# Kernel optimization log

Measured on AMD Instinct MI355X. Metric: run time of the kernel, lower is better.

## Reference

```python
import jax, jax.numpy as jnp
import numpy as np

NEG_SLOPE = 0.01  # torch LeakyReLU default
LN_EPS = 1e-5
L2_EPS = 1e-12  # torch F.normalize eps


def setup_inputs() -> dict:
    key = jax.random.key(0)
    ks = jax.random.split(key, 8)
    B, T, N, C = 16, 32, 64, 256
    local_feat = jax.random.normal(ks[0], (B, T, N, C), dtype=jnp.float32)
    global_feat = jax.random.normal(ks[1], (B, C), dtype=jnp.float32)
    pos = jax.random.normal(ks[2], (B, T * N, 3), dtype=jnp.float32)
    adj_w = jax.random.normal(ks[3], (C, C), dtype=jnp.float32) * (1.0 / np.sqrt(C))
    affine_w = jax.random.normal(ks[4], (C, C), dtype=jnp.float32) * np.sqrt(2.0 / C)  # kaiming-ish
    affine_b = jnp.zeros((C,), dtype=jnp.float32)
    ln_g = jnp.ones((C,), dtype=jnp.float32)
    ln_b = jnp.zeros((C,), dtype=jnp.float32)
    return {"local_feat": local_feat, "global_feat": global_feat, "pos": pos,
            "adj_w": adj_w, "affine_w": affine_w, "affine_b": affine_b,
            "ln_g": ln_g, "ln_b": ln_b}


def reference(local_feat, global_feat, pos, adj_w, affine_w, affine_b, ln_g, ln_b):
    B, T, N, C = local_feat.shape
    x = local_feat.reshape(B, T * N, C)  # [B, M, C]
    # L2 normalize along features
    nrm = jnp.sqrt(jnp.sum(x * x, axis=-1, keepdims=True))
    nf = x / jnp.maximum(nrm, L2_EPS)
    # bilinear scores: A = nf @ W @ nf^T  -> [B, M, M]
    A = jnp.einsum('bnc,cd,bmd->bnm', nf, adj_w, nf)
    A = 5.0 * (A - jnp.max(A, axis=-1, keepdims=True))
    A = jax.nn.softmax(A, axis=-1)
    # affine projection (torch Linear: x @ W^T + b)
    h = jnp.einsum('bmc,dc->bmd', x, affine_w) + affine_b
    # aggregation
    h = jnp.einsum('bnm,bmc->bnc', A, h)
    # LayerNorm + LeakyReLU
    mu = jnp.mean(h, axis=-1, keepdims=True)
    var = jnp.mean(jnp.square(h - mu), axis=-1, keepdims=True)
    h = (h - mu) / jnp.sqrt(var + LN_EPS) * ln_g + ln_b
    h = jnp.where(h >= 0, h, NEG_SLOPE * h)
    return h.reshape(B, T, N, C)
```

## Files before the change

### kernel.cpp

```cpp
#include <hip/hip_runtime.h>
#include <hip/hip_bf16.h>
#include <stdint.h>

#define B_  16
#define M_  2048
#define C_  256
#define BM_ 32768

typedef __bf16 bf16x8 __attribute__((ext_vector_type(8)));
typedef __bf16 bf16x2 __attribute__((ext_vector_type(2)));
typedef float  f32x4  __attribute__((ext_vector_type(4)));
typedef float  f32x16 __attribute__((ext_vector_type(16)));
typedef unsigned int uint2v __attribute__((ext_vector_type(2)));

__device__ __forceinline__ unsigned short f2bf(float f) {
    uint32_t u = __builtin_bit_cast(uint32_t, f);
    u += 0x7fffu + ((u >> 16) & 1u);
    return (unsigned short)(u >> 16);
}

__device__ __forceinline__ uint32_t pkbf(float a, float b) {
    bf16x2 t; t[0] = (__bf16)a; t[1] = (__bf16)b;
    return __builtin_bit_cast(uint32_t, t);
}

__device__ __forceinline__ float bf2f(unsigned short u) {
    return __builtin_bit_cast(float, ((uint32_t)u) << 16);
}

__device__ __forceinline__ void gload16(const void* g, void* l) {
    __builtin_amdgcn_global_load_lds(
        (const __attribute__((address_space(1))) void*)g,
        (__attribute__((address_space(3))) void*)l, 16, 0, 0);
}

__device__ __forceinline__ void publish_barrier() {
    asm volatile("s_waitcnt vmcnt(0)" ::: "memory");
    __builtin_amdgcn_sched_barrier(0);
    __syncthreads();
    __builtin_amdgcn_sched_barrier(0);
}

__global__ void prep_weights(const float* __restrict__ adj,
                             const float* __restrict__ affw,
                             unsigned short* __restrict__ adjT5,
                             unsigned short* __restrict__ affwB) {
    int idx = blockIdx.x * 256 + threadIdx.x;
    int d = idx >> 8, c = idx & 255;
    adjT5[d * 256 + c] = f2bf(7.2134752f * adj[c * 256 + d]);
    affwB[idx] = f2bf(affw[idx]);
}

__global__ void l2norm_kernel(const float* __restrict__ x,
                              unsigned short* __restrict__ nf,
                              float* __restrict__ norms) {
    int w = threadIdx.x >> 6, lane = threadIdx.x & 63;
    int row = blockIdx.x * 4 + w;
    const float4 v = *reinterpret_cast<const float4*>(x + (size_t)row * 256 + lane * 4);
    float ss = v.x * v.x + v.y * v.y + v.z * v.z + v.w * v.w;
    #pragma unroll
    for (int m = 1; m < 64; m <<= 1) ss += __shfl_xor(ss, m);
    float nrm = sqrtf(ss);
    float s = 1.0f / fmaxf(nrm, 1e-12f);
    ushort4 o;
    o.x = f2bf(v.x * s); o.y = f2bf(v.y * s); o.z = f2bf(v.z * s); o.w = f2bf(v.w * s);
    *reinterpret_cast<ushort4*>(nf + (size_t)row * 256 + lane * 4) = o;
    if (lane == 0) norms[row] = nrm;
}

__global__ __launch_bounds__(512, 2)
void dual_gemm(const unsigned short* __restrict__ A,
               const unsigned short* __restrict__ B1,
               const unsigned short* __restrict__ B2,
               const float* __restrict__ norms,
               const float* __restrict__ bias,
               unsigned short* __restrict__ outQ,
               unsigned short* __restrict__ outV3) {
    __shared__ unsigned short bb1[256 * 56];
    __shared__ unsigned short bb2[256 * 56];
    int tid = threadIdx.x;
    int w = tid >> 6, lane = tid & 63, g = lane >> 4, r = lane & 15;
    int m0 = blockIdx.x * 128;

    const f32x4 z = {0.f, 0.f, 0.f, 0.f};
    f32x4 accq[16], accv[16];
    #pragma unroll
    for (int i = 0; i < 16; i++) { accq[i] = z; accv[i] = z; }

    for (int dc = 0; dc < 8; dc++) {
        __syncthreads();
        #pragma unroll
        for (int it = 0; it < 2; it++) {
            int n = (w * 2 + it) * 16 + (lane >> 2);
            int t = lane & 3;
            *reinterpret_cast<uint4*>(&bb1[n * 56 + t * 8]) =
                *reinterpret_cast<const uint4*>(B1 + (size_t)n * 256 + dc * 32 + t * 8);
            *reinterpret_cast<uint4*>(&bb2[n * 56 + t * 8]) =
                *reinterpret_cast<const uint4*>(B2 + (size_t)n * 256 + dc * 32 + t * 8);
        }
        __syncthreads();
        bf16x8 af = *reinterpret_cast<const bf16x8*>(
            A + (size_t)(m0 + w * 16 + r) * 256 + dc * 32 + g * 8);
        #pragma unroll
        for (int nf16 = 0; nf16 < 16; nf16++) {
            bf16x8 b1f = *reinterpret_cast<const bf16x8*>(&bb1[(nf16 * 16 + r) * 56 + g * 8]);
            accq[nf16] = __builtin_amdgcn_mfma_f32_16x16x32_bf16(af, b1f, accq[nf16], 0, 0, 0);
            bf16x8 b2f = *reinterpret_cast<const bf16x8*>(&bb2[(nf16 * 16 + r) * 56 + g * 8]);
            accv[nf16] = __builtin_amdgcn_mfma_f32_16x16x32_bf16(af, b2f, accv[nf16], 0, 0, 0);
        }
    }
    #pragma unroll
    for (int nf16 = 0; nf16 < 16; nf16++) {
        int n = nf16 * 16 + r;
        #pragma unroll
        for (int j = 0; j < 4; j++) {
            int m = m0 + w * 16 + g * 4 + j;
            outQ[(size_t)m * 256 + n] = f2bf(accq[nf16][j]);
        }
    }
    int mm = m0 + w * 16 + g * 4;
    int kvblk = mm >> 5;
    int kv0 = mm & 31;
    int jj  = kv0 >> 4;
    int hl2 = (kv0 >> 3) & 1;
    int e0  = kv0 & 7;
    float4 nr = *reinterpret_cast<const float4*>(norms + mm);
    #pragma unroll
    for (int nf16 = 0; nf16 < 16; nf16++) {
        int n = nf16 * 16 + r;
        int cb = n >> 5, mrow = n & 31;
        int slot = (cb * 2 + jj) * 64 + hl2 * 32 + mrow;
        float bv = bias[n];
        ushort4 o;
        o.x = f2bf(accv[nf16][0] * nr.x + bv);
        o.y = f2bf(accv[nf16][1] * nr.y + bv);
        o.z = f2bf(accv[nf16][2] * nr.z + bv);
        o.w = f2bf(accv[nf16][3] * nr.w + bv);
        *reinterpret_cast<ushort4*>(outV3 + (size_t)kvblk * 8192 + slot * 8 + e0) = o;
    }
}

__global__ __launch_bounds__(512, 1)
void flash_kernel(const unsigned short* __restrict__ Q,
                  const unsigned short* __restrict__ K,
                  const unsigned short* __restrict__ V3,
                  const float* __restrict__ gam,
                  const float* __restrict__ bet,
                  float* __restrict__ out) {
    __shared__ __align__(16) char smem[132096];
    const int tid = threadIdx.x;
    const int w = tid >> 6, lane = tid & 63;
    const int wg = w & 3, h = w >> 2;
    const int hl = lane >> 5, m = lane & 31;
    const int blk = blockIdx.x;
    const int b = (blk & 7) * 2 + (blk >> 7);
    const int mblk = (blk >> 3) & 15;
    const int q0 = b * M_ + mblk * 128 + wg * 32;
    const int gtid = wg * 64 + lane;

    char* gbase = smem + h * 65536;

    bf16x8 qf[16];
    #pragma unroll
    for (int ch = 0; ch < 16; ch++)
        qf[ch] = *reinterpret_cast<const bf16x8*>(
            Q + (size_t)(q0 + m) * 256 + ch * 16 + hl * 8);

    const f32x16 z16 = {0,0,0,0, 0,0,0,0, 0,0,0,0, 0,0,0,0};
    f32x16 acc[8];
    #pragma unroll
    for (int cb = 0; cb < 8; cb++) acc[cb] = z16;
    float mmax = 0.0f, lsum = 0.0f;

    const unsigned short* Kb = K + (size_t)(b * M_ + h * 1024) * 256;
    const unsigned short* Vsrc =
        V3 + ((size_t)(b * 64 + h * 32) * 1024 + gtid) * 8;

    auto stageK = [&](int step, int buf) {
        char* kb = gbase + buf * 16384;
        #pragma unroll
        for (int it = 0; it < 4; it++) {
            int s = it * 256 + gtid;
            int n = s >> 5, t = s & 31;
            gload16(Kb + (size_t)(step * 32 + n) * 256 + ((t ^ (n & 7)) * 8),
                    kb + (it * 256 + wg * 64) * 16);
        }
    };
    auto stageV = [&](int step, int buf) {
        char* vb = gbase + 32768 + buf * 16384;
        const unsigned short* src = Vsrc + (size_t)step * 8192;
        #pragma unroll
        for (int it = 0; it < 4; it++) {
            gload16(src + it * 2048, vb + (it * 256 + wg * 64) * 16);
        }
    };

    stageK(0, 0); stageV(0, 0);
    publish_barrier();
    stageK(1, 1); stageV(1, 1);

    #pragma unroll 2
    for (int step = 0; step < 32; step++) {
        const int cur = step & 1;
        char* kb = gbase + cur * 16384;
        char* vb = gbase + 32768 + cur * 16384;

        f32x16 sf = z16;
        __builtin_amdgcn_s_setprio(1);
        #pragma unroll
        for (int ch = 0; ch < 16; ch++) {
            int slot = (ch * 2 + hl) ^ (m & 7);
            bf16x8 kf = *reinterpret_cast<const bf16x8*>(kb + m * 512 + slot * 16);
            sf = __builtin_amdgcn_mfma_f32_32x32x16_bf16(kf, qf[ch], sf, 0, 0, 0);
        }
        __builtin_amdgcn_s_setprio(0);

        float tm = sf[0];
        #pragma unroll
        for (int i = 1; i < 16; i++) tm = fmaxf(tm, sf[i]);
        tm = fmaxf(tm, __shfl_xor(tm, 32));
        if (__any(tm > mmax + 11.0f)) {
            float mn = fmaxf(mmax, tm);
            float corr = exp2f(mmax - mn);
            lsum *= corr;
            #pragma unroll
            for (int cb = 0; cb < 8; cb++) acc[cb] *= corr;
            mmax = mn;
        }
        #pragma unroll
        for (int i = 0; i < 16; i++) {
            sf[i] = exp2f(sf[i] - mmax);
            lsum += sf[i];
        }
        uint32_t pk0 = pkbf(sf[0], sf[1]),   pk1 = pkbf(sf[2], sf[3]);
        uint32_t pk2 = pkbf(sf[4], sf[5]),   pk3 = pkbf(sf[6], sf[7]);
        uint32_t pk4 = pkbf(sf[8], sf[9]),   pk5 = pkbf(sf[10], sf[11]);
        uint32_t pk6 = pkbf(sf[12], sf[13]), pk7 = pkbf(sf[14], sf[15]);
        uint2v r0 = __builtin_amdgcn_permlane32_swap(pk0, pk2, false, false);
        uint2v r1 = __builtin_amdgcn_permlane32_swap(pk1, pk3, false, false);
        uint2v r2 = __builtin_amdgcn_permlane32_swap(pk4, pk6, false, false);
        uint2v r3 = __builtin_amdgcn_permlane32_swap(pk5, pk7, false, false);
        uint4 u0; u0.x = r0[0]; u0.y = r1[0]; u0.z = r0[1]; u0.w = r1[1];
        uint4 u1; u1.x = r2[0]; u1.y = r3[0]; u1.z = r2[1]; u1.w = r3[1];
        bf16x8 pf0 = __builtin_bit_cast(bf16x8, u0);
        bf16x8 pf1 = __builtin_bit_cast(bf16x8, u1);

        __builtin_amdgcn_s_setprio(1);
        #pragma unroll
        for (int cb = 0; cb < 8; cb++) {
            bf16x8 v0 = *reinterpret_cast<const bf16x8*>(
                vb + lane * 16 + (cb * 2 + 0) * 1024);
            acc[cb] = __builtin_amdgcn_mfma_f32_32x32x16_bf16(v0, pf0, acc[cb], 0, 0, 0);
            bf16x8 v1 = *reinterpret_cast<const bf16x8*>(
                vb + lane * 16 + (cb * 2 + 1) * 1024);
            acc[cb] = __builtin_amdgcn_mfma_f32_32x32x16_bf16(v1, pf1, acc[cb], 0, 0, 0);
        }
        __builtin_amdgcn_s_setprio(0);

        publish_barrier();
        if (step + 2 < 32) {
            stageK(step + 2, cur);
            stageV(step + 2, cur);
        }
    }

    publish_barrier();

    lsum += __shfl_xor(lsum, 32);
    float inv = 1.0f / lsum;
    float wgt = lsum * exp2f(mmax);

    unsigned short* mp = (unsigned short*)smem;
    float* mlp = (float*)(smem + 131072);
    if (h == 1) {
        #pragma unroll
        for (int cb = 0; cb < 8; cb++)
            #pragma unroll
            for (int q4 = 0; q4 < 4; q4++) {
                int c0i = cb * 32 + q4 * 8 + 4 * hl;
                uint2 u;
                u.x = pkbf(acc[cb][q4 * 4 + 0] * inv, acc[cb][q4 * 4 + 1] * inv);
                u.y = pkbf(acc[cb][q4 * 4 + 2] * inv, acc[cb][q4 * 4 + 3] * inv);
                *reinterpret_cast<uint2*>(mp + (size_t)wg * 8192 + m * 256 + c0i) = u;
            }
        if (hl == 0) mlp[wg * 32 + m] = wgt;
    }
    __syncthreads();
    if (h == 0) {
        float w1 = mlp[wg * 32 + m];
        float rsw = 1.0f / (wgt + w1);
        float c0 = wgt * rsw * inv;
        float c1 = w1 * rsw;
        float s = 0.0f, ssq = 0.0f;
        #pragma unroll
        for (int cb = 0; cb < 8; cb++)
            #pragma unroll
            for (int q4 = 0; q4 < 4; q4++) {
                int c0i = cb * 32 + q4 * 8 + 4 * hl;
                uint2 u = *reinterpret_cast<const uint2*>(
                    mp + (size_t)wg * 8192 + m * 256 + c0i);
                float p0 = bf2f((unsigned short)(u.x & 0xffff));
                float p1 = bf2f((unsigned short)(u.x >> 16));
                float p2 = bf2f((unsigned short)(u.y & 0xffff));
                float p3 = bf2f((unsigned short)(u.y >> 16));
                float v0 = acc[cb][q4 * 4 + 0] * c0 + p0 * c1;
                float v1 = acc[cb][q4 * 4 + 1] * c0 + p1 * c1;
                float v2 = acc[cb][q4 * 4 + 2] * c0 + p2 * c1;
                float v3 = acc[cb][q4 * 4 + 3] * c0 + p3 * c1;
                acc[cb][q4 * 4 + 0] = v0; acc[cb][q4 * 4 + 1] = v1;
                acc[cb][q4 * 4 + 2] = v2; acc[cb][q4 * 4 + 3] = v3;
                s += (v0 + v1) + (v2 + v3);
                ssq += v0 * v0 + v1 * v1 + v2 * v2 + v3 * v3;
            }
        s   += __shfl_xor(s, 32);
        ssq += __shfl_xor(ssq, 32);
        float mu = s * (1.0f / 256.0f);
        float var = ssq * (1.0f / 256.0f) - mu * mu;
        float rstd = rsqrtf(var + 1e-5f);
        size_t rowoff = (size_t)(q0 + m) * 256;
        #pragma unroll
        for (int cb = 0; cb < 8; cb++)
            #pragma unroll
            for (int q4 = 0; q4 < 4; q4++) {
                int c0i = cb * 32 + q4 * 8 + 4 * hl;
                float4 gg = *reinterpret_cast<const float4*>(gam + c0i);
                float4 bb = *reinterpret_cast<const float4*>(bet + c0i);
                float4 o;
                o.x = (acc[cb][q4 * 4 + 0] - mu) * rstd * gg.x + bb.x;
                o.y = (acc[cb][q4 * 4 + 1] - mu) * rstd * gg.y + bb.y;
                o.z = (acc[cb][q4 * 4 + 2] - mu) * rstd * gg.z + bb.z;
                o.w = (acc[cb][q4 * 4 + 3] - mu) * rstd * gg.w + bb.w;
                o.x = o.x >= 0.f ? o.x : 0.01f * o.x;
                o.y = o.y >= 0.f ? o.y : 0.01f * o.y;
                o.z = o.z >= 0.f ? o.z : 0.01f * o.z;
                o.w = o.w >= 0.f ? o.w : 0.01f * o.w;
                *reinterpret_cast<float4*>(out + rowoff + c0i) = o;
            }
    }
}

extern "C" void kernel_launch(void* const* d_in, const int* in_sizes, int n_in,
                              void* d_out, int out_size, void* d_ws, size_t ws_size,
                              hipStream_t stream) {
    const float* local_feat = (const float*)d_in[0];
    const float* adj_w    = (const float*)d_in[3];
    const float* affine_w = (const float*)d_in[4];
    const float* affine_b = (const float*)d_in[5];
    const float* ln_g     = (const float*)d_in[6];
    const float* ln_b     = (const float*)d_in[7];
    float* out = (float*)d_out;

    char* ws = (char*)d_ws;
    unsigned short* nf    = (unsigned short*)(ws);
    unsigned short* q     = (unsigned short*)(ws + 16777216);
    unsigned short* v3    = (unsigned short*)(ws + 33554432);
    float*          norms = (float*)         (ws + 50331648);
    unsigned short* adjT5 = (unsigned short*)(ws + 50462720);
    unsigned short* affw  = (unsigned short*)(ws + 50593792);

    prep_weights<<<256, 256, 0, stream>>>(adj_w, affine_w, adjT5, affw);
    l2norm_kernel<<<BM_ / 4, 256, 0, stream>>>(local_feat, nf, norms);
    dual_gemm<<<BM_ / 128, 512, 0, stream>>>(nf, adjT5, affw, norms, affine_b, q, v3);
    flash_kernel<<<256, 512, 0, stream>>>(q, nf, v3, ln_g, ln_b, out);
}
```

Measured before the change: 137.0 us.

## Pre-swizzle K into MFMA fragment layout in dual_gemm for linear LDS reads

dual_gemm now writes an extra copy of the normalized features (K) in a blocked fragment layout matching the V3 layout. The flash kernel stages K with the same contiguous per-lane 16-byte loads as V and reads K fragments from LDS with a simple lane*16 + ch*1024 offset, dropping the XOR swizzle address math. The main loop's unroll-2 pragma is also removed. This costs an extra 16 MB global write in dual_gemm, and the new LDS read pattern could bring back bank conflicts.

```diff
diff --git a/kernel.cpp b/kernel.cpp
--- a/kernel.cpp
+++ b/kernel.cpp
@@ -75,7 +75,8 @@
                const float* __restrict__ norms,
                const float* __restrict__ bias,
                unsigned short* __restrict__ outQ,
-               unsigned short* __restrict__ outV3) {
+               unsigned short* __restrict__ outV3,
+               unsigned short* __restrict__ outK3) {
     __shared__ unsigned short bb1[256 * 56];
     __shared__ unsigned short bb2[256 * 56];
     int tid = threadIdx.x;
@@ -86,6 +87,9 @@
     f32x4 accq[16], accv[16];
     #pragma unroll
     for (int i = 0; i < 16; i++) { accq[i] = z; accv[i] = z; }
+
+    int row = m0 + w * 16 + r;
+    int kvblk_r = row >> 5, mrow = row & 31;
 
     for (int dc = 0; dc < 8; dc++) {
         __syncthreads();
@@ -100,7 +104,13 @@
         }
         __syncthreads();
         bf16x8 af = *reinterpret_cast<const bf16x8*>(
-            A + (size_t)(m0 + w * 16 + r) * 256 + dc * 32 + g * 8);
+            A + (size_t)row * 256 + dc * 32 + g * 8);
+        {
+            int ch = dc * 2 + (g >> 1);
+            int khl = g & 1;
+            *reinterpret_cast<bf16x8*>(
+                outK3 + (size_t)kvblk_r * 8192 + ch * 512 + (khl * 32 + mrow) * 8) = af;
+        }
         #pragma unroll
         for (int nf16 = 0; nf16 < 16; nf16++) {
             bf16x8 b1f = *reinterpret_cast<const bf16x8*>(&bb1[(nf16 * 16 + r) * 56 + g * 8]);
@@ -128,8 +138,8 @@
     #pragma unroll
     for (int nf16 = 0; nf16 < 16; nf16++) {
         int n = nf16 * 16 + r;
-        int cb = n >> 5, mrow = n & 31;
-        int slot = (cb * 2 + jj) * 64 + hl2 * 32 + mrow;
+        int cb = n >> 5, mr2 = n & 31;
+        int slot = (cb * 2 + jj) * 64 + hl2 * 32 + mr2;
         float bv = bias[n];
         ushort4 o;
         o.x = f2bf(accv[nf16][0] * nr.x + bv);
@@ -142,7 +152,7 @@
 
 __global__ __launch_bounds__(512, 1)
 void flash_kernel(const unsigned short* __restrict__ Q,
-                  const unsigned short* __restrict__ K,
+                  const unsigned short* __restrict__ K3,
                   const unsigned short* __restrict__ V3,
                   const float* __restrict__ gam,
                   const float* __restrict__ bet,
@@ -172,45 +182,40 @@
     for (int cb = 0; cb < 8; cb++) acc[cb] = z16;
     float mmax = 0.0f, lsum = 0.0f;
 
-    const unsigned short* Kb = K + (size_t)(b * M_ + h * 1024) * 256;
+    const unsigned short* Ksrc =
+        K3 + ((size_t)(b * 64 + h * 32) * 1024 + gtid) * 8;
     const unsigned short* Vsrc =
         V3 + ((size_t)(b * 64 + h * 32) * 1024 + gtid) * 8;
 
     auto stageK = [&](int step, int buf) {
         char* kb = gbase + buf * 16384;
-        #pragma unroll
-        for (int it = 0; it < 4; it++) {
-            int s = it * 256 + gtid;
-            int n = s >> 5, t = s & 31;
-            gload16(Kb + (size_t)(step * 32 + n) * 256 + ((t ^ (n & 7)) * 8),
-                    kb + (it * 256 + wg * 64) * 16);
-        }
+        const unsigned short* src = Ksrc + (size_t)step * 8192;
+        #pragma unroll
+        for (int it = 0; it < 4; it++)
+            gload16(src + it * 2048, kb + (it * 256 + wg * 64) * 16);
     };
     auto stageV = [&](int step, int buf) {
         char* vb = gbase + 32768 + buf * 16384;
         const unsigned short* src = Vsrc + (size_t)step * 8192;
         #pragma unroll
-        for (int it = 0; it < 4; it++) {
+        for (int it = 0; it < 4; it++)
             gload16(src + it * 2048, vb + (it * 256 + wg * 64) * 16);
-        }
     };
 
     stageK(0, 0); stageV(0, 0);
     publish_barrier();
     stageK(1, 1); stageV(1, 1);
 
-    #pragma unroll 2
     for (int step = 0; step < 32; step++) {
         const int cur = step & 1;
-        char* kb = gbase + cur * 16384;
-        char* vb = gbase + 32768 + cur * 16384;
+        const char* kbl = gbase + cur * 16384 + lane * 16;
+        const char* vbl = gbase + 32768 + cur * 16384 + lane * 16;
 
         f32x16 sf = z16;
         __builtin_amdgcn_s_setprio(1);
         #pragma unroll
         for (int ch = 0; ch < 16; ch++) {
-            int slot = (ch * 2 + hl) ^ (m & 7);
-            bf16x8 kf = *reinterpret_cast<const bf16x8*>(kb + m * 512 + slot * 16);
+            bf16x8 kf = *reinterpret_cast<const bf16x8*>(kbl + ch * 1024);
             sf = __builtin_amdgcn_mfma_f32_32x32x16_bf16(kf, qf[ch], sf, 0, 0, 0);
         }
         __builtin_amdgcn_s_setprio(0);
@@ -248,11 +253,9 @@
         __builtin_amdgcn_s_setprio(1);
         #pragma unroll
         for (int cb = 0; cb < 8; cb++) {
-            bf16x8 v0 = *reinterpret_cast<const bf16x8*>(
-                vb + lane * 16 + (cb * 2 + 0) * 1024);
+            bf16x8 v0 = *reinterpret_cast<const bf16x8*>(vbl + (cb * 2 + 0) * 1024);
             acc[cb] = __builtin_amdgcn_mfma_f32_32x32x16_bf16(v0, pf0, acc[cb], 0, 0, 0);
-            bf16x8 v1 = *reinterpret_cast<const bf16x8*>(
-                vb + lane * 16 + (cb * 2 + 1) * 1024);
+            bf16x8 v1 = *reinterpret_cast<const bf16x8*>(vbl + (cb * 2 + 1) * 1024);
             acc[cb] = __builtin_amdgcn_mfma_f32_32x32x16_bf16(v1, pf1, acc[cb], 0, 0, 0);
         }
         __builtin_amdgcn_s_setprio(0);
@@ -357,9 +360,10 @@
     float*          norms = (float*)         (ws + 50331648);
     unsigned short* adjT5 = (unsigned short*)(ws + 50462720);
     unsigned short* affw  = (unsigned short*)(ws + 50593792);
+    unsigned short* k3    = (unsigned short*)(ws + 50724864);
 
     prep_weights<<<256, 256, 0, stream>>>(adj_w, affine_w, adjT5, affw);
     l2norm_kernel<<<BM_ / 4, 256, 0, stream>>>(local_feat, nf, norms);
-    dual_gemm<<<BM_ / 128, 512, 0, stream>>>(nf, adjT5, affw, norms, affine_b, q, v3);
-    flash_kernel<<<256, 512, 0, stream>>>(q, nf, v3, ln_g, ln_b, out);
-}
+    dual_gemm<<<BM_ / 128, 512, 0, stream>>>(nf, adjT5, affw, norms, affine_b, q, v3, k3);
+    flash_kernel<<<256, 512, 0, stream>>>(q, k3, v3, ln_g, ln_b, out);
+}
```

After: 131.2 us. 4.2% less time.
